# Performance work log

Hardware: AMD Instinct MI355X
Metric: run time of the kernel (lower is better)

Reference implementation:

```python
import jax, jax.numpy as jnp
import numpy as np

N, K, A, LOCAL, PAIR = 1024, 48, 5, 512, 128
RBF_BINS = 16

def _normalize(v, eps=1e-8):
    return v / jnp.sqrt(jnp.sum(v * v, axis=-1, keepdims=True) + eps)

def _frames(pos):
    # pos: (N, A, 3); backbone frame from N(0), CA(1), C(2) via Gram-Schmidt
    n, ca, c = pos[:, 0], pos[:, 1], pos[:, 2]
    e1 = _normalize(c - ca)
    v2 = n - ca
    e2 = _normalize(v2 - jnp.sum(v2 * e1, -1, keepdims=True) * e1)
    e3 = jnp.cross(e1, e2)
    R = jnp.stack([e1, e2, e3], axis=-1)  # (N,3,3) columns are frame axes
    return R, ca

def _rbf(d, d_min=0.0, d_max=22.0, bins=RBF_BINS):
    centers = jnp.linspace(d_min, d_max, bins)
    step = (d_max - d_min) / bins
    return jnp.exp(-((d[..., None] - centers) / step) ** 2)

def setup_inputs():
    key = jax.random.key(0)
    ks = jax.random.split(key, 16)
    def rn(k, shape, scale=1.0):
        return (scale * jax.random.normal(k, shape)).astype(jnp.float32)
    local = rn(ks[0], (N, LOCAL))
    pos = rn(ks[1], (N, A, 3), 3.0)
    pair = rn(ks[2], (N, N, PAIR), 0.1)
    neighbours = jax.random.randint(ks[3], (N, K), 0, N).astype(jnp.int32)
    mask = jnp.ones((N,), dtype=bool)
    d_dist = A * A * RBF_BINS   # 400
    d_dir = A * A * 3           # 75
    d_vec = 2 * A * 3           # 30
    s = lambda f: 1.0 / np.sqrt(f)
    return dict(
        local=local, pos=pos, pair=pair, neighbours=neighbours, mask=mask,
        W_li=rn(ks[4], (LOCAL, PAIR), s(LOCAL)),
        W_lj=rn(ks[5], (LOCAL, PAIR), s(LOCAL)),
        W_dist=rn(ks[6], (d_dist, PAIR), s(d_dist)),
        W_dir=rn(ks[7], (d_dir, PAIR), s(d_dir)),
        W_rot=rn(ks[8], (9, PAIR), s(9)),
        W_vec=rn(ks[9], (d_vec, PAIR), s(d_vec)),
        ln_scale=jnp.ones((PAIR,), jnp.float32),
        ln_bias=jnp.zeros((PAIR,), jnp.float32),
        mlp_w1=rn(ks[10], (PAIR, 2 * PAIR), s(PAIR)),
        mlp_b1=jnp.zeros((2 * PAIR,), jnp.float32),
        mlp_w2=rn(ks[11], (2 * PAIR, PAIR), s(2 * PAIR)),
        mlp_b2=jnp.zeros((PAIR,), jnp.float32),
    )

def reference(local, pos, pair, neighbours, mask,
              W_li, W_lj, W_dist, W_dir, W_rot, W_vec,
              ln_scale, ln_bias, mlp_w1, mlp_b1, mlp_w2, mlp_b2):
    n_idx = jnp.arange(neighbours.shape[0])
    pair_mask = (mask[:, None] & mask[neighbours]) & (neighbours != -1)
    p = pair[n_idx[:, None], neighbours]                      # (N,K,PAIR) gather
    R, t = _frames(pos)                                       # (N,3,3), (N,3)
    pos_nb = pos[neighbours]                                  # (N,K,A,3)
    # source / target node feature projections
    p = p + (local @ W_li)[:, None] + (local @ W_lj)[neighbours]
    # distance features: all atom-pair distances, RBF-encoded in [0, 22]
    off = pos[:, None, :, None, :] - pos_nb[:, :, None, :, :] # (N,K,A,A,3)
    dist = jnp.sqrt(jnp.sum(off * off, -1) + 1e-8)            # (N,K,A,A)
    p = p + _rbf(dist).reshape(*neighbours.shape, -1) @ W_dist
    # direction features: atom-pair offsets in the local frame, normalized
    off_local = jnp.einsum('nij,nkabi->nkabj', R, off)
    p = p + _normalize(off_local).reshape(*neighbours.shape, -1) @ W_dir
    # relative rotation features: R_i^T R_j, flattened
    R_rel = jnp.einsum('nai,nkaj->nkij', R, R[neighbours])
    p = p + R_rel.reshape(*neighbours.shape, 9) @ W_rot
    # pair vector features: self and neighbour atoms in the local frame (x0.1)
    x_self = jnp.einsum('nij,nai->naj', R, pos - t[:, None])            # (N,A,3)
    x_nb = jnp.einsum('nij,nkai->nkaj', R, pos_nb - t[:, None, None])   # (N,K,A,3)
    vec = jnp.concatenate(
        (0.1 * jnp.broadcast_to(x_self[:, None], x_nb.shape), 0.1 * x_nb),
        axis=-1).reshape(*neighbours.shape, -1)
    p = p + vec @ W_vec
    # LayerNorm (scale + offset)
    mu = jnp.mean(p, -1, keepdims=True)
    var = jnp.var(p, -1, keepdims=True)
    p = (p - mu) * jax.lax.rsqrt(var + 1e-5) * ln_scale + ln_bias
    # MLP: hidden 2*PAIR, gelu, linear out
    p = jax.nn.gelu(p @ mlp_w1 + mlp_b1) @ mlp_w2 + mlp_b2
    return p, pair_mask
```

## Files before the change

### kernel.cpp

```cpp
#include <hip/hip_runtime.h>
#include <hip/hip_bf16.h>
#include <math.h>

#define N 1024
#define K 48
#define A 5
#define LOCALD 512
#define PAIRD 128
#define ROWS 32
#define FEATK 544
#define SF_STRIDE_B 1152

#define WS_LI (N*9 + N*3 + N*15)
#define WS_LJ (WS_LI + N*128)
#define WCT_OFF 1159168u
#define W1T_OFF 1298432u
#define W2T_OFF 1363968u
#define PA_OFF  1429504u
#define WS_NEEDED (1429504ull + 49152ull*128*2)

typedef _Float16 half8 __attribute__((ext_vector_type(8)));
typedef float f32x16 __attribute__((ext_vector_type(16)));

__device__ __forceinline__ float gelu_fast(float x) {
    float u2 = 1.5957691216057308f * x * (1.0f + 0.044715f * x * x);
    float t = __expf(-u2);
    return x * __builtin_amdgcn_rcpf(1.0f + t);
}

__device__ __forceinline__ void frame_from(const float* __restrict__ P, float* __restrict__ R) {
    float e1x = P[6] - P[3], e1y = P[7] - P[4], e1z = P[8] - P[5];
    float inv1 = rsqrtf(e1x * e1x + e1y * e1y + e1z * e1z + 1e-8f);
    e1x *= inv1; e1y *= inv1; e1z *= inv1;
    float v2x = P[0] - P[3], v2y = P[1] - P[4], v2z = P[2] - P[5];
    float dp = v2x * e1x + v2y * e1y + v2z * e1z;
    float e2x = v2x - dp * e1x, e2y = v2y - dp * e1y, e2z = v2z - dp * e1z;
    float inv2 = rsqrtf(e2x * e2x + e2y * e2y + e2z * e2z + 1e-8f);
    e2x *= inv2; e2y *= inv2; e2z *= inv2;
    float e3x = e1y * e2z - e1z * e2y;
    float e3y = e1z * e2x - e1x * e2z;
    float e3z = e1x * e2y - e1y * e2x;
    R[0] = e1x; R[1] = e2x; R[2] = e3x;
    R[3] = e1y; R[4] = e2y; R[5] = e3y;
    R[6] = e1z; R[7] = e2z; R[8] = e3z;
}

__global__ __launch_bounds__(256) void prep_kernel(
    const float* __restrict__ local_,
    const float* __restrict__ W_li, const float* __restrict__ W_lj,
    const float* __restrict__ Wd, const float* __restrict__ Wdir,
    const float* __restrict__ Wrot, const float* __restrict__ Wv,
    const float* __restrict__ w1, const float* __restrict__ w2,
    float* __restrict__ ws, char* __restrict__ wsb)
{
    const int tid = threadIdx.x;
    if (blockIdx.x >= 256) {
        _Float16* wct = (_Float16*)(wsb + WCT_OFF);
        _Float16* w1t = (_Float16*)(wsb + W1T_OFF);
        _Float16* w2t = (_Float16*)(wsb + W2T_OFF);
        int g = (blockIdx.x - 256) * 256 + tid;
        if (g < 128 * 544) {
            int c = g & 127, f = g >> 7;
            float v = 0.0f;
            if (f < 400) v = Wd[(size_t)f * 128 + c];
            else if (f < 475) v = Wdir[(size_t)(f - 400) * 128 + c];
            else if (f < 484) v = Wrot[(size_t)(f - 475) * 128 + c];
            else if (f < 514) v = Wv[(size_t)(f - 484) * 128 + c];
            wct[(size_t)c * FEATK + f] = (_Float16)v;
        } else {
            int g2 = g - 128 * 544;
            if (g2 < 256 * 128) {
                int c = g2 & 255, f = g2 >> 8;
                w1t[(size_t)c * 128 + f] = (_Float16)w1[(size_t)f * 256 + c];
            } else {
                int g3 = g2 - 256 * 128;
                if (g3 < 128 * 256) {
                    int c = g3 & 127, f = g3 >> 7;
                    w2t[(size_t)c * 256 + f] = (_Float16)w2[(size_t)f * 128 + c];
                }
            }
        }
        return;
    }

    const int n0 = blockIdx.x * 4;
    __shared__ float sl[4][LOCALD];
    for (int t = tid; t < 4 * LOCALD; t += 256) {
        int r = t >> 9, q = t & 511;
        sl[r][q] = local_[(size_t)(n0 + r) * LOCALD + q];
    }
    __syncthreads();

    const int c = tid & 127;
    const int hh = tid >> 7;
    const int r0 = hh * 2;
    float ali0 = 0, ali1 = 0, alj0 = 0, alj1 = 0;
    const float* wli = W_li + c;
    const float* wlj = W_lj + c;
    #pragma unroll 8
    for (int f = 0; f < LOCALD; ++f) {
        float a_ = wli[(size_t)f * 128];
        float b_ = wlj[(size_t)f * 128];
        float l0 = sl[r0 + 0][f], l1 = sl[r0 + 1][f];
        ali0 += l0 * a_; ali1 += l1 * a_;
        alj0 += l0 * b_; alj1 += l1 * b_;
    }
    ws[WS_LI + (size_t)(n0 + r0 + 0) * 128 + c] = ali0;
    ws[WS_LI + (size_t)(n0 + r0 + 1) * 128 + c] = ali1;
    ws[WS_LJ + (size_t)(n0 + r0 + 0) * 128 + c] = alj0;
    ws[WS_LJ + (size_t)(n0 + r0 + 1) * 128 + c] = alj1;
}

__device__ __forceinline__ void sfw(char* smem, int r, int f, float v) {
    int off = r * SF_STRIDE_B + ((f * 2) ^ ((r & 7) << 4));
    *(_Float16*)(smem + off) = (_Float16)v;
}

template<bool SPLIT>
__global__ __launch_bounds__(256, 4) void main_kernel(
    const float* __restrict__ pair, const float* __restrict__ pos,
    const int* __restrict__ neigh, const int* __restrict__ mask,
    const float* __restrict__ ln_s, const float* __restrict__ ln_b,
    const float* __restrict__ b1, const float* __restrict__ b2,
    const float* __restrict__ ws, const char* __restrict__ wsb,
    _Float16* __restrict__ pa, float* __restrict__ out)
{
    const int R0 = blockIdx.x * ROWS;
    const int tid = threadIdx.x;
    const int lane = tid & 63;
    const int wv = tid >> 6;
    const int myrow = lane & 31;
    const int hi = lane >> 5;
    const int khalf = hi * 8;
    const int swz = (myrow & 7) << 4;

    __shared__ __align__(16) char smem[40960];
    int*   sn  = (int*)(smem + 36864);
    int*   sj  = (int*)(smem + 36992);
    float* spn = (float*)(smem + 37120);
    float* spj = (float*)(smem + 39040);

    const _Float16* wct = (const _Float16*)(wsb + WCT_OFF);
    const int colbase = wv * 32 + myrow;

    if (tid < ROWS) {
        int Rg = R0 + tid;
        int n = Rg / K;
        int kk = Rg - n * K;
        int j = neigh[n * K + kk];
        if (j < 0) j += N;
        sn[tid] = n; sj[tid] = j;
    }
    __syncthreads();

    const int nb0 = R0 / K;
    const int nb1 = (nb0 + 1 < N) ? nb0 + 1 : nb0;
    float li0 = ws[WS_LI + (size_t)nb0 * PAIRD + colbase];
    float li1 = ws[WS_LI + (size_t)nb1 * PAIRD + colbase];
    float pv[16];
    #pragma unroll
    for (int q = 0; q < 16; ++q) {
        int rr = (q & 3) + 8 * (q >> 2) + 4 * hi;
        int nq = sn[rr], jq = sj[rr];
        float li = (nq == nb0) ? li0 : li1;
        pv[q] = pair[((size_t)nq * N + jq) * PAIRD + colbase]
              + ws[WS_LJ + (size_t)jq * PAIRD + colbase] + li;
    }

    for (int t = tid; t < ROWS * 15; t += 256) {
        int r = t / 15, q = t % 15;
        spn[t] = pos[(size_t)sn[r] * 15 + q];
        spj[t] = pos[(size_t)sj[r] * 15 + q];
    }
    __syncthreads();

    {
        const int fr  = tid >> 3;
        const int sub = tid & 7;
        const float* Pn = spn + fr * 15;
        const float* Pj = spj + fr * 15;

        sfw(smem, fr, 514 + sub, 0.0f);
        sfw(smem, fr, 522 + sub, 0.0f);
        sfw(smem, fr, 530 + sub, 0.0f);
        if (sub < 6) sfw(smem, fr, 538 + sub, 0.0f);

        float rn[9];
        frame_from(Pn, rn);

        #pragma unroll
        for (int m = 0; m < 4; ++m) {
            int ab = sub + 8 * m;
            if (ab < 25) {
                int a = ab / 5, b = ab - 5 * (ab / 5);
                float o0 = Pn[a * 3 + 0] - Pj[b * 3 + 0];
                float o1 = Pn[a * 3 + 1] - Pj[b * 3 + 1];
                float o2 = Pn[a * 3 + 2] - Pj[b * 3 + 2];
                float d = sqrtf(o0 * o0 + o1 * o1 + o2 * o2 + 1e-8f);
                float z = d * (16.0f / 22.0f);
                int base = a * 80 + b * 16;
                int rb = fr * SF_STRIDE_B;
                int rsw = (fr & 7) << 4;
                #pragma unroll
                for (int bp = 0; bp < 8; ++bp) {
                    float e0 = __expf(-z * z);
                    float z1 = z - 1.0666666666666667f;
                    float e1 = __expf(-z1 * z1);
                    z = z1 - 1.0666666666666667f;
                    union { _Float16 h[2]; unsigned u; } pk;
                    pk.h[0] = (_Float16)e0; pk.h[1] = (_Float16)e1;
                    int off = rb + (((base + bp * 2) * 2) ^ rsw);
                    *(unsigned*)(smem + off) = pk.u;
                }
                float l0 = rn[0] * o0 + rn[3] * o1 + rn[6] * o2;
                float l1 = rn[1] * o0 + rn[4] * o1 + rn[7] * o2;
                float l2 = rn[2] * o0 + rn[5] * o1 + rn[8] * o2;
                float inv = rsqrtf(l0 * l0 + l1 * l1 + l2 * l2 + 1e-8f);
                int dbase = 400 + a * 15 + b * 3;
                sfw(smem, fr, dbase + 0, l0 * inv);
                sfw(smem, fr, dbase + 1, l1 * inv);
                sfw(smem, fr, dbase + 2, l2 * inv);
            }
        }

        #pragma unroll
        for (int m = 0; m < 2; ++m) {
            int task = (m == 0) ? sub : (sub < 2 ? 8 + sub : -1);
            if (task >= 0) {
                int a = task >> 1;
                int kind = task & 1;
                const float* Ps = kind ? Pj : Pn;
                float v0 = Ps[a * 3 + 0] - Pn[3];
                float v1 = Ps[a * 3 + 1] - Pn[4];
                float v2 = Ps[a * 3 + 2] - Pn[5];
                float x0 = rn[0] * v0 + rn[3] * v1 + rn[6] * v2;
                float x1 = rn[1] * v0 + rn[4] * v1 + rn[7] * v2;
                float x2 = rn[2] * v0 + rn[5] * v1 + rn[8] * v2;
                int dbase = 484 + a * 6 + kind * 3;
                sfw(smem, fr, dbase + 0, 0.1f * x0);
                sfw(smem, fr, dbase + 1, 0.1f * x1);
                sfw(smem, fr, dbase + 2, 0.1f * x2);
            }
        }

        if (sub == 7) {
            float rj[9];
            frame_from(Pj, rj);
            #pragma unroll
            for (int i = 0; i < 3; ++i)
                #pragma unroll
                for (int jd = 0; jd < 3; ++jd) {
                    float v = rn[0 * 3 + i] * rj[0 * 3 + jd]
                            + rn[1 * 3 + i] * rj[1 * 3 + jd]
                            + rn[2 * 3 + i] * rj[2 * 3 + jd];
                    sfw(smem, fr, 475 + i * 3 + jd, v);
                }
        }
    }
    __syncthreads();

    f32x16 acc0, acc1;
    #pragma unroll
    for (int q = 0; q < 16; ++q) { acc0[q] = 0.0f; acc1[q] = 0.0f; }
    {
        const _Float16* wp = wct + (size_t)colbase * FEATK + khalf;
        #pragma unroll
        for (int ks = 0; ks < 34; ks += 2) {
            half8 b0 = *(const half8*)(wp + ks * 16);
            half8 b1 = *(const half8*)(wp + (ks + 1) * 16);
            int k0 = ks * 16 + khalf;
            int k1 = (ks + 1) * 16 + khalf;
            half8 a0 = *(const half8*)(smem + myrow * SF_STRIDE_B + ((k0 * 2) ^ swz));
            half8 a1 = *(const half8*)(smem + myrow * SF_STRIDE_B + ((k1 * 2) ^ swz));
            acc0 = __builtin_amdgcn_mfma_f32_32x32x16_f16(a0, b0, acc0, 0, 0, 0);
            acc1 = __builtin_amdgcn_mfma_f32_32x32x16_f16(a1, b1, acc1, 0, 0, 0);
        }
    }
    __syncthreads();

    #pragma unroll
    for (int q = 0; q < 16; ++q) {
        int rr = (q & 3) + 8 * (q >> 2) + 4 * hi;
        *(float*)(smem + rr * 512 + colbase * 4) = acc0[q] + acc1[q] + pv[q];
    }
    __syncthreads();

    {
        float lns0 = ln_s[lane], lns1 = ln_s[lane + 64];
        float lnb0 = ln_b[lane], lnb1 = ln_b[lane + 64];
        #pragma unroll
        for (int rr8 = 0; rr8 < 8; ++rr8) {
            int row = wv * 8 + rr8;
            float v0 = *(float*)(smem + row * 512 + lane * 4);
            float v1 = *(float*)(smem + row * 512 + (lane + 64) * 4);
            float s = v0 + v1, s2 = v0 * v0 + v1 * v1;
            #pragma unroll
            for (int o = 32; o > 0; o >>= 1) {
                s += __shfl_xor(s, o, 64);
                s2 += __shfl_xor(s2, o, 64);
            }
            float mu = s * (1.0f / 128.0f);
            float var = s2 * (1.0f / 128.0f) - mu * mu;
            float rs = rsqrtf(var + 1e-5f);
            float y0 = (v0 - mu) * rs * lns0 + lnb0;
            float y1 = (v1 - mu) * rs * lns1 + lnb1;
            if constexpr (SPLIT) {
                pa[(size_t)(R0 + row) * PAIRD + lane]      = (_Float16)y0;
                pa[(size_t)(R0 + row) * PAIRD + lane + 64] = (_Float16)y1;
            } else {
                int sw = (row & 7) << 4;
                *(_Float16*)(smem + 16384 + row * 256 + ((lane * 2) ^ sw)) = (_Float16)y0;
                *(_Float16*)(smem + 16384 + row * 256 + (((lane + 64) * 2) ^ sw)) = (_Float16)y1;
            }
        }
    }
    if constexpr (SPLIT) return;

    __syncthreads();

    {
        const _Float16* w1t = (const _Float16*)(wsb + W1T_OFF);
        const int c0 = wv * 64 + myrow;
        const int c1 = c0 + 32;
        const _Float16* wp0 = w1t + (size_t)c0 * 128 + khalf;
        const _Float16* wp1 = w1t + (size_t)c1 * 128 + khalf;
        f32x16 h0, h1;
        #pragma unroll
        for (int q = 0; q < 16; ++q) { h0[q] = 0.0f; h1[q] = 0.0f; }
        #pragma unroll
        for (int ks = 0; ks < 8; ++ks) {
            half8 wf0 = *(const half8*)(wp0 + ks * 16);
            half8 wf1 = *(const half8*)(wp1 + ks * 16);
            int k0 = ks * 16 + khalf;
            half8 a = *(const half8*)(smem + 16384 + myrow * 256 + ((k0 * 2) ^ swz));
            h0 = __builtin_amdgcn_mfma_f32_32x32x16_f16(a, wf0, h0, 0, 0, 0);
            h1 = __builtin_amdgcn_mfma_f32_32x32x16_f16(a, wf1, h1, 0, 0, 0);
        }
        float bb0 = b1[c0], bb1 = b1[c1];
        #pragma unroll
        for (int q = 0; q < 16; ++q) {
            int rr = (q & 3) + 8 * (q >> 2) + 4 * hi;
            int sw = (rr & 7) << 4;
            *(_Float16*)(smem + rr * 512 + ((c0 * 2) ^ sw)) = (_Float16)gelu_fast(h0[q] + bb0);
            *(_Float16*)(smem + rr * 512 + ((c1 * 2) ^ sw)) = (_Float16)gelu_fast(h1[q] + bb1);
        }
    }
    __syncthreads();

    {
        const _Float16* w2t = (const _Float16*)(wsb + W2T_OFF);
        const int oc = wv * 32 + myrow;
        const _Float16* wp = w2t + (size_t)oc * 256 + khalf;
        f32x16 o0, o1;
        #pragma unroll
        for (int q = 0; q < 16; ++q) { o0[q] = 0.0f; o1[q] = 0.0f; }
        #pragma unroll
        for (int ks = 0; ks < 16; ks += 2) {
            half8 w0 = *(const half8*)(wp + ks * 16);
            half8 w1f = *(const half8*)(wp + (ks + 1) * 16);
            int k0 = ks * 16 + khalf;
            int k1 = (ks + 1) * 16 + khalf;
            half8 a0 = *(const half8*)(smem + myrow * 512 + ((k0 * 2) ^ swz));
            half8 a1 = *(const half8*)(smem + myrow * 512 + ((k1 * 2) ^ swz));
            o0 = __builtin_amdgcn_mfma_f32_32x32x16_f16(a0, w0, o0, 0, 0, 0);
            o1 = __builtin_amdgcn_mfma_f32_32x32x16_f16(a1, w1f, o1, 0, 0, 0);
        }
        float bb = b2[oc];
        #pragma unroll
        for (int q = 0; q < 16; ++q) {
            int rr = (q & 3) + 8 * (q >> 2) + 4 * hi;
            out[((size_t)(R0 + rr)) * PAIRD + oc] = o0[q] + o1[q] + bb;
        }
    }

    if (tid < ROWS) {
        int Rg = R0 + tid;
        int n = Rg / K;
        int kk = Rg - n * K;
        int jr = neigh[n * K + kk];
        int jj = jr < 0 ? jr + N : jr;
        bool pm = (jr != -1) && (mask[n] != 0) && (mask[jj] != 0);
        out[(size_t)N * K * PAIRD + Rg] = pm ? 1.0f : 0.0f;
    }
}

__global__ __launch_bounds__(256, 3) void mlp_kernel(
    const _Float16* __restrict__ pa, const int* __restrict__ neigh,
    const int* __restrict__ mask, const float* __restrict__ b1,
    const float* __restrict__ b2, const char* __restrict__ wsb,
    float* __restrict__ out)
{
    const int R0 = blockIdx.x * 64;
    const int tid = threadIdx.x;
    const int lane = tid & 63;
    const int wv = tid >> 6;
    const int myrow = lane & 31;
    const int hi = lane >> 5;
    const int khalf = hi * 8;
    const int swz = (myrow & 7) << 4;

    __shared__ __align__(16) char smem[49152];

    for (int ch = tid; ch < 1024; ch += 256) {
        int row = ch >> 4, c16 = ch & 15;
        half8 v = *(const half8*)(pa + (size_t)(R0 + row) * PAIRD + c16 * 8);
        *(half8*)(smem + row * 256 + ((c16 * 16) ^ ((row & 7) << 4))) = v;
    }
    __syncthreads();

    {
        const _Float16* w1t = (const _Float16*)(wsb + W1T_OFF);
        const int c0 = wv * 64 + myrow;
        const int c1 = c0 + 32;
        const _Float16* wp0 = w1t + (size_t)c0 * 128 + khalf;
        const _Float16* wp1 = w1t + (size_t)c1 * 128 + khalf;
        f32x16 h00, h01, h10, h11;
        #pragma unroll
        for (int q = 0; q < 16; ++q) { h00[q] = 0.0f; h01[q] = 0.0f; h10[q] = 0.0f; h11[q] = 0.0f; }
        #pragma unroll
        for (int ks = 0; ks < 8; ++ks) {
            int k0 = ks * 16 + khalf;
            half8 wf0 = *(const half8*)(wp0 + ks * 16);
            half8 wf1 = *(const half8*)(wp1 + ks * 16);
            half8 a0 = *(const half8*)(smem + myrow * 256 + ((k0 * 2) ^ swz));
            half8 a1 = *(const half8*)(smem + (32 + myrow) * 256 + ((k0 * 2) ^ swz));
            h00 = __builtin_amdgcn_mfma_f32_32x32x16_f16(a0, wf0, h00, 0, 0, 0);
            h01 = __builtin_amdgcn_mfma_f32_32x32x16_f16(a0, wf1, h01, 0, 0, 0);
            h10 = __builtin_amdgcn_mfma_f32_32x32x16_f16(a1, wf0, h10, 0, 0, 0);
            h11 = __builtin_amdgcn_mfma_f32_32x32x16_f16(a1, wf1, h11, 0, 0, 0);
        }
        float bb0 = b1[c0], bb1 = b1[c1];
        #pragma unroll
        for (int q = 0; q < 16; ++q) {
            int rr = (q & 3) + 8 * (q >> 2) + 4 * hi;
            int sw = (rr & 7) << 4;
            *(_Float16*)(smem + 16384 + rr * 512 + ((c0 * 2) ^ sw)) = (_Float16)gelu_fast(h00[q] + bb0);
            *(_Float16*)(smem + 16384 + rr * 512 + ((c1 * 2) ^ sw)) = (_Float16)gelu_fast(h01[q] + bb1);
            *(_Float16*)(smem + 16384 + (rr + 32) * 512 + ((c0 * 2) ^ sw)) = (_Float16)gelu_fast(h10[q] + bb0);
            *(_Float16*)(smem + 16384 + (rr + 32) * 512 + ((c1 * 2) ^ sw)) = (_Float16)gelu_fast(h11[q] + bb1);
        }
    }
    __syncthreads();

    {
        const _Float16* w2t = (const _Float16*)(wsb + W2T_OFF);
        const int oc = wv * 32 + myrow;
        const _Float16* wp = w2t + (size_t)oc * 256 + khalf;
        f32x16 o0, o1;
        #pragma unroll
        for (int q = 0; q < 16; ++q) { o0[q] = 0.0f; o1[q] = 0.0f; }
        #pragma unroll
        for (int ks = 0; ks < 16; ++ks) {
            int k0 = ks * 16 + khalf;
            half8 wf = *(const half8*)(wp + ks * 16);
            half8 a0 = *(const half8*)(smem + 16384 + myrow * 512 + ((k0 * 2) ^ swz));
            half8 a1 = *(const half8*)(smem + 16384 + (32 + myrow) * 512 + ((k0 * 2) ^ swz));
            o0 = __builtin_amdgcn_mfma_f32_32x32x16_f16(a0, wf, o0, 0, 0, 0);
            o1 = __builtin_amdgcn_mfma_f32_32x32x16_f16(a1, wf, o1, 0, 0, 0);
        }
        float bb = b2[oc];
        #pragma unroll
        for (int q = 0; q < 16; ++q) {
            int rr = (q & 3) + 8 * (q >> 2) + 4 * hi;
            out[((size_t)(R0 + rr)) * PAIRD + oc]      = o0[q] + bb;
            out[((size_t)(R0 + rr + 32)) * PAIRD + oc] = o1[q] + bb;
        }
    }

    if (tid < 64) {
        int Rg = R0 + tid;
        int n = Rg / K;
        int kk = Rg - n * K;
        int jr = neigh[n * K + kk];
        int jj = jr < 0 ? jr + N : jr;
        bool pm = (jr != -1) && (mask[n] != 0) && (mask[jj] != 0);
        out[(size_t)N * K * PAIRD + Rg] = pm ? 1.0f : 0.0f;
    }
}

extern "C" void kernel_launch(void* const* d_in, const int* in_sizes, int n_in,
                              void* d_out, int out_size, void* d_ws, size_t ws_size,
                              hipStream_t stream) {
    const float* local_ = (const float*)d_in[0];
    const float* pos = (const float*)d_in[1];
    const float* pair = (const float*)d_in[2];
    const int* neigh = (const int*)d_in[3];
    const int* mask = (const int*)d_in[4];
    const float* W_li = (const float*)d_in[5];
    const float* W_lj = (const float*)d_in[6];
    const float* W_dist = (const float*)d_in[7];
    const float* W_dir = (const float*)d_in[8];
    const float* W_rot = (const float*)d_in[9];
    const float* W_vec = (const float*)d_in[10];
    const float* ln_s = (const float*)d_in[11];
    const float* ln_b = (const float*)d_in[12];
    const float* w1 = (const float*)d_in[13];
    const float* b1 = (const float*)d_in[14];
    const float* w2 = (const float*)d_in[15];
    const float* b2 = (const float*)d_in[16];
    float* ws = (float*)d_ws;
    char* wsb = (char*)d_ws;
    _Float16* pa = (_Float16*)(wsb + PA_OFF);
    float* out = (float*)d_out;

    hipLaunchKernelGGL(prep_kernel, dim3(256 + 528), dim3(256), 0, stream,
                       local_, W_li, W_lj, W_dist, W_dir, W_rot, W_vec,
                       w1, w2, ws, wsb);
    if (ws_size >= WS_NEEDED) {
        main_kernel<true><<<dim3((N * K) / ROWS), dim3(256), 0, stream>>>(
            pair, pos, neigh, mask, ln_s, ln_b, b1, b2, ws, wsb, pa, out);
        mlp_kernel<<<dim3((N * K) / 64), dim3(256), 0, stream>>>(
            pa, neigh, mask, b1, b2, wsb, out);
    } else {
        main_kernel<false><<<dim3((N * K) / ROWS), dim3(256), 0, stream>>>(
            pair, pos, neigh, mask, ln_s, ln_b, b1, b2, ws, wsb, pa, out);
    }
}
```

Measured before the change: 80.09 us.

## Keep weight fragments in registers and loop blocks over multiple row tiles

Both the feature-projection kernel and the MLP kernel now load their weight fragments into registers once per block and then process several row tiles in a loop (3 tiles for main, 2 for mlp). Grid sizes shrink to match. This removes repeated global/L2 reads of the weights for every 32/64-row tile. In exchange it uses many more VGPRs (34 half8 fragments in main), so main_kernel's launch bound drops to 2 blocks per CU, and fewer, longer blocks reduce latency hiding and parallelism.

```diff
diff --git a/kernel.cpp b/kernel.cpp
--- a/kernel.cpp
+++ b/kernel.cpp
@@ -8,6 +8,8 @@
 #define LOCALD 512
 #define PAIRD 128
 #define ROWS 32
+#define TPB 3
+#define MTPB 2
 #define FEATK 544
 #define SF_STRIDE_B 1152
 
@@ -117,7 +119,7 @@
 }
 
 template<bool SPLIT>
-__global__ __launch_bounds__(256, 4) void main_kernel(
+__global__ __launch_bounds__(256, 2) void main_kernel(
     const float* __restrict__ pair, const float* __restrict__ pos,
     const int* __restrict__ neigh, const int* __restrict__ mask,
     const float* __restrict__ ln_s, const float* __restrict__ ln_b,
@@ -125,7 +127,6 @@
     const float* __restrict__ ws, const char* __restrict__ wsb,
     _Float16* __restrict__ pa, float* __restrict__ out)
 {
-    const int R0 = blockIdx.x * ROWS;
     const int tid = threadIdx.x;
     const int lane = tid & 63;
     const int wv = tid >> 6;
@@ -140,257 +141,270 @@
     float* spn = (float*)(smem + 37120);
     float* spj = (float*)(smem + 39040);
 
-    const _Float16* wct = (const _Float16*)(wsb + WCT_OFF);
     const int colbase = wv * 32 + myrow;
 
-    if (tid < ROWS) {
-        int Rg = R0 + tid;
-        int n = Rg / K;
-        int kk = Rg - n * K;
-        int j = neigh[n * K + kk];
-        if (j < 0) j += N;
-        sn[tid] = n; sj[tid] = j;
-    }
-    __syncthreads();
-
-    const int nb0 = R0 / K;
-    const int nb1 = (nb0 + 1 < N) ? nb0 + 1 : nb0;
-    float li0 = ws[WS_LI + (size_t)nb0 * PAIRD + colbase];
-    float li1 = ws[WS_LI + (size_t)nb1 * PAIRD + colbase];
-    float pv[16];
-    #pragma unroll
-    for (int q = 0; q < 16; ++q) {
-        int rr = (q & 3) + 8 * (q >> 2) + 4 * hi;
-        int nq = sn[rr], jq = sj[rr];
-        float li = (nq == nb0) ? li0 : li1;
-        pv[q] = pair[((size_t)nq * N + jq) * PAIRD + colbase]
-              + ws[WS_LJ + (size_t)jq * PAIRD + colbase] + li;
-    }
-
-    for (int t = tid; t < ROWS * 15; t += 256) {
-        int r = t / 15, q = t % 15;
-        spn[t] = pos[(size_t)sn[r] * 15 + q];
-        spj[t] = pos[(size_t)sj[r] * 15 + q];
-    }
-    __syncthreads();
-
+    half8 bw[34];
     {
-        const int fr  = tid >> 3;
-        const int sub = tid & 7;
-        const float* Pn = spn + fr * 15;
-        const float* Pj = spj + fr * 15;
-
-        sfw(smem, fr, 514 + sub, 0.0f);
-        sfw(smem, fr, 522 + sub, 0.0f);
-        sfw(smem, fr, 530 + sub, 0.0f);
-        if (sub < 6) sfw(smem, fr, 538 + sub, 0.0f);
-
-        float rn[9];
-        frame_from(Pn, rn);
-
-        #pragma unroll
-        for (int m = 0; m < 4; ++m) {
-            int ab = sub + 8 * m;
-            if (ab < 25) {
-                int a = ab / 5, b = ab - 5 * (ab / 5);
-                float o0 = Pn[a * 3 + 0] - Pj[b * 3 + 0];
-                float o1 = Pn[a * 3 + 1] - Pj[b * 3 + 1];
-                float o2 = Pn[a * 3 + 2] - Pj[b * 3 + 2];
-                float d = sqrtf(o0 * o0 + o1 * o1 + o2 * o2 + 1e-8f);
-                float z = d * (16.0f / 22.0f);
-                int base = a * 80 + b * 16;
-                int rb = fr * SF_STRIDE_B;
-                int rsw = (fr & 7) << 4;
+        const _Float16* wp = (const _Float16*)(wsb + WCT_OFF) + (size_t)colbase * FEATK + khalf;
+        #pragma unroll
+        for (int ks = 0; ks < 34; ++ks)
+            bw[ks] = *(const half8*)(wp + ks * 16);
+    }
+
+    for (int tile = 0; tile < TPB; ++tile) {
+        const int R0 = (blockIdx.x * TPB + tile) * ROWS;
+        __syncthreads();
+
+        if (tid < ROWS) {
+            int Rg = R0 + tid;
+            int n = Rg / K;
+            int kk = Rg - n * K;
+            int j = neigh[n * K + kk];
+            if (j < 0) j += N;
+            sn[tid] = n; sj[tid] = j;
+        }
+        __syncthreads();
+
+        const int nb0 = R0 / K;
+        const int nb1 = (nb0 + 1 < N) ? nb0 + 1 : nb0;
+        float li0 = ws[WS_LI + (size_t)nb0 * PAIRD + colbase];
+        float li1 = ws[WS_LI + (size_t)nb1 * PAIRD + colbase];
+        float pv[16];
+        #pragma unroll
+        for (int q = 0; q < 16; ++q) {
+            int rr = (q & 3) + 8 * (q >> 2) + 4 * hi;
+            int nq = sn[rr], jq = sj[rr];
+            float li = (nq == nb0) ? li0 : li1;
+            pv[q] = pair[((size_t)nq * N + jq) * PAIRD + colbase]
+                  + ws[WS_LJ + (size_t)jq * PAIRD + colbase] + li;
+        }
+
+        for (int t = tid; t < ROWS * 15; t += 256) {
+            int r = t / 15, q = t % 15;
+            spn[t] = pos[(size_t)sn[r] * 15 + q];
+            spj[t] = pos[(size_t)sj[r] * 15 + q];
+        }
+        __syncthreads();
+
+        {
+            const int fr  = tid >> 3;
+            const int sub = tid & 7;
+            const float* Pn = spn + fr * 15;
+            const float* Pj = spj + fr * 15;
+
+            sfw(smem, fr, 514 + sub, 0.0f);
+            sfw(smem, fr, 522 + sub, 0.0f);
+            sfw(smem, fr, 530 + sub, 0.0f);
+            if (sub < 6) sfw(smem, fr, 538 + sub, 0.0f);
+
+            float rn[9];
+            frame_from(Pn, rn);
+
+            #pragma unroll
+            for (int m = 0; m < 4; ++m) {
+                int ab = sub + 8 * m;
+                if (ab < 25) {
+                    int a = ab / 5, b = ab - 5 * (ab / 5);
+                    float o0 = Pn[a * 3 + 0] - Pj[b * 3 + 0];
+                    float o1 = Pn[a * 3 + 1] - Pj[b * 3 + 1];
+                    float o2 = Pn[a * 3 + 2] - Pj[b * 3 + 2];
+                    float d = sqrtf(o0 * o0 + o1 * o1 + o2 * o2 + 1e-8f);
+                    float z = d * (16.0f / 22.0f);
+                    int base = a * 80 + b * 16;
+                    int rb = fr * SF_STRIDE_B;
+                    int rsw = (fr & 7) << 4;
+                    #pragma unroll
+                    for (int bp = 0; bp < 8; ++bp) {
+                        float e0 = __expf(-z * z);
+                        float z1 = z - 1.0666666666666667f;
+                        float e1 = __expf(-z1 * z1);
+                        z = z1 - 1.0666666666666667f;
+                        union { _Float16 h[2]; unsigned u; } pk;
+                        pk.h[0] = (_Float16)e0; pk.h[1] = (_Float16)e1;
+                        int off = rb + (((base + bp * 2) * 2) ^ rsw);
+                        *(unsigned*)(smem + off) = pk.u;
+                    }
+                    float l0 = rn[0] * o0 + rn[3] * o1 + rn[6] * o2;
+                    float l1 = rn[1] * o0 + rn[4] * o1 + rn[7] * o2;
+                    float l2 = rn[2] * o0 + rn[5] * o1 + rn[8] * o2;
+                    float inv = rsqrtf(l0 * l0 + l1 * l1 + l2 * l2 + 1e-8f);
+                    int dbase = 400 + a * 15 + b * 3;
+                    sfw(smem, fr, dbase + 0, l0 * inv);
+                    sfw(smem, fr, dbase + 1, l1 * inv);
+                    sfw(smem, fr, dbase + 2, l2 * inv);
+                }
+            }
+
+            #pragma unroll
+            for (int m = 0; m < 2; ++m) {
+                int task = (m == 0) ? sub : (sub < 2 ? 8 + sub : -1);
+                if (task >= 0) {
+                    int a = task >> 1;
+                    int kind = task & 1;
+                    const float* Ps = kind ? Pj : Pn;
+                    float v0 = Ps[a * 3 + 0] - Pn[3];
+                    float v1 = Ps[a * 3 + 1] - Pn[4];
+                    float v2 = Ps[a * 3 + 2] - Pn[5];
+                    float x0 = rn[0] * v0 + rn[3] * v1 + rn[6] * v2;
+                    float x1 = rn[1] * v0 + rn[4] * v1 + rn[7] * v2;
+                    float x2 = rn[2] * v0 + rn[5] * v1 + rn[8] * v2;
+                    int dbase = 484 + a * 6 + kind * 3;
+                    sfw(smem, fr, dbase + 0, 0.1f * x0);
+                    sfw(smem, fr, dbase + 1, 0.1f * x1);
+                    sfw(smem, fr, dbase + 2, 0.1f * x2);
+                }
+            }
+
+            if (sub == 7) {
+                float rj[9];
+                frame_from(Pj, rj);
                 #pragma unroll
-                for (int bp = 0; bp < 8; ++bp) {
-                    float e0 = __expf(-z * z);
-                    float z1 = z - 1.0666666666666667f;
-                    float e1 = __expf(-z1 * z1);
-                    z = z1 - 1.0666666666666667f;
-                    union { _Float16 h[2]; unsigned u; } pk;
-                    pk.h[0] = (_Float16)e0; pk.h[1] = (_Float16)e1;
-                    int off = rb + (((base + bp * 2) * 2) ^ rsw);
-                    *(unsigned*)(smem + off) = pk.u;
-                }
-                float l0 = rn[0] * o0 + rn[3] * o1 + rn[6] * o2;
-                float l1 = rn[1] * o0 + rn[4] * o1 + rn[7] * o2;
-                float l2 = rn[2] * o0 + rn[5] * o1 + rn[8] * o2;
-                float inv = rsqrtf(l0 * l0 + l1 * l1 + l2 * l2 + 1e-8f);
-                int dbase = 400 + a * 15 + b * 3;
-                sfw(smem, fr, dbase + 0, l0 * inv);
-                sfw(smem, fr, dbase + 1, l1 * inv);
-                sfw(smem, fr, dbase + 2, l2 * inv);
-            }
-        }
-
-        #pragma unroll
-        for (int m = 0; m < 2; ++m) {
-            int task = (m == 0) ? sub : (sub < 2 ? 8 + sub : -1);
-            if (task >= 0) {
-                int a = task >> 1;
-                int kind = task & 1;
-                const float* Ps = kind ? Pj : Pn;
-                float v0 = Ps[a * 3 + 0] - Pn[3];
-                float v1 = Ps[a * 3 + 1] - Pn[4];
-                float v2 = Ps[a * 3 + 2] - Pn[5];
-                float x0 = rn[0] * v0 + rn[3] * v1 + rn[6] * v2;
-                float x1 = rn[1] * v0 + rn[4] * v1 + rn[7] * v2;
-                float x2 = rn[2] * v0 + rn[5] * v1 + rn[8] * v2;
-                int dbase = 484 + a * 6 + kind * 3;
-                sfw(smem, fr, dbase + 0, 0.1f * x0);
-                sfw(smem, fr, dbase + 1, 0.1f * x1);
-                sfw(smem, fr, dbase + 2, 0.1f * x2);
-            }
-        }
-
-        if (sub == 7) {
-            float rj[9];
-            frame_from(Pj, rj);
-            #pragma unroll
-            for (int i = 0; i < 3; ++i)
-                #pragma unroll
-                for (int jd = 0; jd < 3; ++jd) {
-                    float v = rn[0 * 3 + i] * rj[0 * 3 + jd]
-                            + rn[1 * 3 + i] * rj[1 * 3 + jd]
-                            + rn[2 * 3 + i] * rj[2 * 3 + jd];
-                    sfw(smem, fr, 475 + i * 3 + jd, v);
-                }
-        }
-    }
-    __syncthreads();
-
-    f32x16 acc0, acc1;
-    #pragma unroll
-    for (int q = 0; q < 16; ++q) { acc0[q] = 0.0f; acc1[q] = 0.0f; }
-    {
-        const _Float16* wp = wct + (size_t)colbase * FEATK + khalf;
+                for (int i = 0; i < 3; ++i)
+                    #pragma unroll
+                    for (int jd = 0; jd < 3; ++jd) {
+                        float v = rn[0 * 3 + i] * rj[0 * 3 + jd]
+                                + rn[1 * 3 + i] * rj[1 * 3 + jd]
+                                + rn[2 * 3 + i] * rj[2 * 3 + jd];
+                        sfw(smem, fr, 475 + i * 3 + jd, v);
+                    }
+            }
+        }
+        __syncthreads();
+
+        f32x16 acc0, acc1;
+        #pragma unroll
+        for (int q = 0; q < 16; ++q) { acc0[q] = 0.0f; acc1[q] = 0.0f; }
         #pragma unroll
         for (int ks = 0; ks < 34; ks += 2) {
-            half8 b0 = *(const half8*)(wp + ks * 16);
-            half8 b1 = *(const half8*)(wp + (ks + 1) * 16);
             int k0 = ks * 16 + khalf;
             int k1 = (ks + 1) * 16 + khalf;
             half8 a0 = *(const half8*)(smem + myrow * SF_STRIDE_B + ((k0 * 2) ^ swz));
             half8 a1 = *(const half8*)(smem + myrow * SF_STRIDE_B + ((k1 * 2) ^ swz));
-            acc0 = __builtin_amdgcn_mfma_f32_32x32x16_f16(a0, b0, acc0, 0, 0, 0);
-            acc1 = __builtin_amdgcn_mfma_f32_32x32x16_f16(a1, b1, acc1, 0, 0, 0);
-        }
-    }
-    __syncthreads();
-
-    #pragma unroll
-    for (int q = 0; q < 16; ++q) {
-        int rr = (q & 3) + 8 * (q >> 2) + 4 * hi;
-        *(float*)(smem + rr * 512 + colbase * 4) = acc0[q] + acc1[q] + pv[q];
-    }
-    __syncthreads();
-
-    {
-        float lns0 = ln_s[lane], lns1 = ln_s[lane + 64];
-        float lnb0 = ln_b[lane], lnb1 = ln_b[lane + 64];
-        #pragma unroll
-        for (int rr8 = 0; rr8 < 8; ++rr8) {
-            int row = wv * 8 + rr8;
-            float v0 = *(float*)(smem + row * 512 + lane * 4);
-            float v1 = *(float*)(smem + row * 512 + (lane + 64) * 4);
-            float s = v0 + v1, s2 = v0 * v0 + v1 * v1;
-            #pragma unroll
-            for (int o = 32; o > 0; o >>= 1) {
-                s += __shfl_xor(s, o, 64);
-                s2 += __shfl_xor(s2, o, 64);
-            }
-            float mu = s * (1.0f / 128.0f);
-            float var = s2 * (1.0f / 128.0f) - mu * mu;
-            float rs = rsqrtf(var + 1e-5f);
-            float y0 = (v0 - mu) * rs * lns0 + lnb0;
-            float y1 = (v1 - mu) * rs * lns1 + lnb1;
-            if constexpr (SPLIT) {
-                pa[(size_t)(R0 + row) * PAIRD + lane]      = (_Float16)y0;
-                pa[(size_t)(R0 + row) * PAIRD + lane + 64] = (_Float16)y1;
-            } else {
-                int sw = (row & 7) << 4;
-                *(_Float16*)(smem + 16384 + row * 256 + ((lane * 2) ^ sw)) = (_Float16)y0;
-                *(_Float16*)(smem + 16384 + row * 256 + (((lane + 64) * 2) ^ sw)) = (_Float16)y1;
-            }
-        }
-    }
-    if constexpr (SPLIT) return;
-
-    __syncthreads();
-
-    {
-        const _Float16* w1t = (const _Float16*)(wsb + W1T_OFF);
-        const int c0 = wv * 64 + myrow;
-        const int c1 = c0 + 32;
-        const _Float16* wp0 = w1t + (size_t)c0 * 128 + khalf;
-        const _Float16* wp1 = w1t + (size_t)c1 * 128 + khalf;
-        f32x16 h0, h1;
-        #pragma unroll
-        for (int q = 0; q < 16; ++q) { h0[q] = 0.0f; h1[q] = 0.0f; }
-        #pragma unroll
-        for (int ks = 0; ks < 8; ++ks) {
-            half8 wf0 = *(const half8*)(wp0 + ks * 16);
-            half8 wf1 = *(const half8*)(wp1 + ks * 16);
-            int k0 = ks * 16 + khalf;
-            half8 a = *(const half8*)(smem + 16384 + myrow * 256 + ((k0 * 2) ^ swz));
-            h0 = __builtin_amdgcn_mfma_f32_32x32x16_f16(a, wf0, h0, 0, 0, 0);
-            h1 = __builtin_amdgcn_mfma_f32_32x32x16_f16(a, wf1, h1, 0, 0, 0);
-        }
-        float bb0 = b1[c0], bb1 = b1[c1];
+            acc0 = __builtin_amdgcn_mfma_f32_32x32x16_f16(a0, bw[ks], acc0, 0, 0, 0);
+            acc1 = __builtin_amdgcn_mfma_f32_32x32x16_f16(a1, bw[ks + 1], acc1, 0, 0, 0);
+        }
+        __syncthreads();
+
         #pragma unroll
         for (int q = 0; q < 16; ++q) {
             int rr = (q & 3) + 8 * (q >> 2) + 4 * hi;
-            int sw = (rr & 7) << 4;
-            *(_Float16*)(smem + rr * 512 + ((c0 * 2) ^ sw)) = (_Float16)gelu_fast(h0[q] + bb0);
-            *(_Float16*)(smem + rr * 512 + ((c1 * 2) ^ sw)) = (_Float16)gelu_fast(h1[q] + bb1);
-        }
-    }
-    __syncthreads();
-
-    {
-        const _Float16* w2t = (const _Float16*)(wsb + W2T_OFF);
-        const int oc = wv * 32 + myrow;
-        const _Float16* wp = w2t + (size_t)oc * 256 + khalf;
-        f32x16 o0, o1;
-        #pragma unroll
-        for (int q = 0; q < 16; ++q) { o0[q] = 0.0f; o1[q] = 0.0f; }
-        #pragma unroll
-        for (int ks = 0; ks < 16; ks += 2) {
-            half8 w0 = *(const half8*)(wp + ks * 16);
-            half8 w1f = *(const half8*)(wp + (ks + 1) * 16);
-            int k0 = ks * 16 + khalf;
-            int k1 = (ks + 1) * 16 + khalf;
-            half8 a0 = *(const half8*)(smem + myrow * 512 + ((k0 * 2) ^ swz));
-            half8 a1 = *(const half8*)(smem + myrow * 512 + ((k1 * 2) ^ swz));
-            o0 = __builtin_amdgcn_mfma_f32_32x32x16_f16(a0, w0, o0, 0, 0, 0);
-            o1 = __builtin_amdgcn_mfma_f32_32x32x16_f16(a1, w1f, o1, 0, 0, 0);
-        }
-        float bb = b2[oc];
-        #pragma unroll
-        for (int q = 0; q < 16; ++q) {
-            int rr = (q & 3) + 8 * (q >> 2) + 4 * hi;
-            out[((size_t)(R0 + rr)) * PAIRD + oc] = o0[q] + o1[q] + bb;
-        }
-    }
-
-    if (tid < ROWS) {
-        int Rg = R0 + tid;
-        int n = Rg / K;
-        int kk = Rg - n * K;
-        int jr = neigh[n * K + kk];
-        int jj = jr < 0 ? jr + N : jr;
-        bool pm = (jr != -1) && (mask[n] != 0) && (mask[jj] != 0);
-        out[(size_t)N * K * PAIRD + Rg] = pm ? 1.0f : 0.0f;
-    }
-}
-
-__global__ __launch_bounds__(256, 3) void mlp_kernel(
+            *(float*)(smem + rr * 512 + colbase * 4) = acc0[q] + acc1[q] + pv[q];
+        }
+        __syncthreads();
+
+        {
+            float lns0 = ln_s[lane], lns1 = ln_s[lane + 64];
+            float lnb0 = ln_b[lane], lnb1 = ln_b[lane + 64];
+            #pragma unroll
+            for (int rr8 = 0; rr8 < 8; ++rr8) {
+                int row = wv * 8 + rr8;
+                float v0 = *(float*)(smem + row * 512 + lane * 4);
+                float v1 = *(float*)(smem + row * 512 + (lane + 64) * 4);
+                float s = v0 + v1, s2 = v0 * v0 + v1 * v1;
+                #pragma unroll
+                for (int o = 32; o > 0; o >>= 1) {
+                    s += __shfl_xor(s, o, 64);
+                    s2 += __shfl_xor(s2, o, 64);
+                }
+                float mu = s * (1.0f / 128.0f);
+                float var = s2 * (1.0f / 128.0f) - mu * mu;
+                float rs = rsqrtf(var + 1e-5f);
+                float y0 = (v0 - mu) * rs * lns0 + lnb0;
+                float y1 = (v1 - mu) * rs * lns1 + lnb1;
+                if constexpr (SPLIT) {
+                    *(_Float16*)(smem + 16384 + row * 256 + lane * 2) = (_Float16)y0;
+                    *(_Float16*)(smem + 16384 + row * 256 + (lane + 64) * 2) = (_Float16)y1;
+                } else {
+                    int sw = (row & 7) << 4;
+                    *(_Float16*)(smem + 16384 + row * 256 + ((lane * 2) ^ sw)) = (_Float16)y0;
+                    *(_Float16*)(smem + 16384 + row * 256 + (((lane + 64) * 2) ^ sw)) = (_Float16)y1;
+                }
+            }
+        }
+        __syncthreads();
+
+        if constexpr (SPLIT) {
+            for (int ch = tid; ch < ROWS * 16; ch += 256) {
+                int row = ch >> 4, c16 = ch & 15;
+                half8 v = *(const half8*)(smem + 16384 + row * 256 + c16 * 16);
+                *(half8*)(pa + (size_t)(R0 + row) * PAIRD + c16 * 8) = v;
+            }
+            continue;
+        }
+
+        {
+            const _Float16* w1t = (const _Float16*)(wsb + W1T_OFF);
+            const int c0 = wv * 64 + myrow;
+            const int c1 = c0 + 32;
+            const _Float16* wp0 = w1t + (size_t)c0 * 128 + khalf;
+            const _Float16* wp1 = w1t + (size_t)c1 * 128 + khalf;
+            f32x16 h0, h1;
+            #pragma unroll
+            for (int q = 0; q < 16; ++q) { h0[q] = 0.0f; h1[q] = 0.0f; }
+            #pragma unroll
+            for (int ks = 0; ks < 8; ++ks) {
+                half8 wf0 = *(const half8*)(wp0 + ks * 16);
+                half8 wf1 = *(const half8*)(wp1 + ks * 16);
+                int k0 = ks * 16 + khalf;
+                half8 a = *(const half8*)(smem + 16384 + myrow * 256 + ((k0 * 2) ^ swz));
+                h0 = __builtin_amdgcn_mfma_f32_32x32x16_f16(a, wf0, h0, 0, 0, 0);
+                h1 = __builtin_amdgcn_mfma_f32_32x32x16_f16(a, wf1, h1, 0, 0, 0);
+            }
+            float bb0 = b1[c0], bb1 = b1[c1];
+            #pragma unroll
+            for (int q = 0; q < 16; ++q) {
+                int rr = (q & 3) + 8 * (q >> 2) + 4 * hi;
+                int sw = (rr & 7) << 4;
+                *(_Float16*)(smem + rr * 512 + ((c0 * 2) ^ sw)) = (_Float16)gelu_fast(h0[q] + bb0);
+                *(_Float16*)(smem + rr * 512 + ((c1 * 2) ^ sw)) = (_Float16)gelu_fast(h1[q] + bb1);
+            }
+        }
+        __syncthreads();
+
+        {
+            const _Float16* w2t = (const _Float16*)(wsb + W2T_OFF);
+            const int oc = wv * 32 + myrow;
+            const _Float16* wp = w2t + (size_t)oc * 256 + khalf;
+            f32x16 o0, o1;
+            #pragma unroll
+            for (int q = 0; q < 16; ++q) { o0[q] = 0.0f; o1[q] = 0.0f; }
+            #pragma unroll
+            for (int ks = 0; ks < 16; ks += 2) {
+                half8 w0 = *(const half8*)(wp + ks * 16);
+                half8 w1f = *(const half8*)(wp + (ks + 1) * 16);
+                int k0 = ks * 16 + khalf;
+                int k1 = (ks + 1) * 16 + khalf;
+                half8 a0 = *(const half8*)(smem + myrow * 512 + ((k0 * 2) ^ swz));
+                half8 a1 = *(const half8*)(smem + myrow * 512 + ((k1 * 2) ^ swz));
+                o0 = __builtin_amdgcn_mfma_f32_32x32x16_f16(a0, w0, o0, 0, 0, 0);
+                o1 = __builtin_amdgcn_mfma_f32_32x32x16_f16(a1, w1f, o1, 0, 0, 0);
+            }
+            float bb = b2[oc];
+            #pragma unroll
+            for (int q = 0; q < 16; ++q) {
+                int rr = (q & 3) + 8 * (q >> 2) + 4 * hi;
+                out[((size_t)(R0 + rr)) * PAIRD + oc] = o0[q] + o1[q] + bb;
+            }
+        }
+
+        if (tid < ROWS) {
+            int Rg = R0 + tid;
+            int n = Rg / K;
+            int kk = Rg - n * K;
+            int jr = neigh[n * K + kk];
+            int jj = jr < 0 ? jr + N : jr;
+            bool pm = (jr != -1) && (mask[n] != 0) && (mask[jj] != 0);
+            out[(size_t)N * K * PAIRD + Rg] = pm ? 1.0f : 0.0f;
+        }
+    }
+}
+
+__global__ __launch_bounds__(256, 2) void mlp_kernel(
     const _Float16* __restrict__ pa, const int* __restrict__ neigh,
     const int* __restrict__ mask, const float* __restrict__ b1,
     const float* __restrict__ b2, const char* __restrict__ wsb,
     float* __restrict__ out)
 {
-    const int R0 = blockIdx.x * 64;
     const int tid = threadIdx.x;
     const int lane = tid & 63;
     const int wv = tid >> 6;
@@ -401,80 +415,93 @@
 
     __shared__ __align__(16) char smem[49152];
 
-    for (int ch = tid; ch < 1024; ch += 256) {
-        int row = ch >> 4, c16 = ch & 15;
-        half8 v = *(const half8*)(pa + (size_t)(R0 + row) * PAIRD + c16 * 8);
-        *(half8*)(smem + row * 256 + ((c16 * 16) ^ ((row & 7) << 4))) = v;
-    }
-    __syncthreads();
-
+    const int c0 = wv * 64 + myrow;
+    const int c1 = c0 + 32;
+    const int oc = wv * 32 + myrow;
+    half8 wf0[8], wf1[8], w2f[16];
     {
         const _Float16* w1t = (const _Float16*)(wsb + W1T_OFF);
-        const int c0 = wv * 64 + myrow;
-        const int c1 = c0 + 32;
+        const _Float16* w2t = (const _Float16*)(wsb + W2T_OFF);
         const _Float16* wp0 = w1t + (size_t)c0 * 128 + khalf;
         const _Float16* wp1 = w1t + (size_t)c1 * 128 + khalf;
-        f32x16 h00, h01, h10, h11;
-        #pragma unroll
-        for (int q = 0; q < 16; ++q) { h00[q] = 0.0f; h01[q] = 0.0f; h10[q] = 0.0f; h11[q] = 0.0f; }
+        const _Float16* wp2 = w2t + (size_t)oc * 256 + khalf;
         #pragma unroll
         for (int ks = 0; ks < 8; ++ks) {
-            int k0 = ks * 16 + khalf;
-            half8 wf0 = *(const half8*)(wp0 + ks * 16);
-            half8 wf1 = *(const half8*)(wp1 + ks * 16);
-            half8 a0 = *(const half8*)(smem + myrow * 256 + ((k0 * 2) ^ swz));
-            half8 a1 = *(const half8*)(smem + (32 + myrow) * 256 + ((k0 * 2) ^ swz));
-            h00 = __builtin_amdgcn_mfma_f32_32x32x16_f16(a0, wf0, h00, 0, 0, 0);
-            h01 = __builtin_amdgcn_mfma_f32_32x32x16_f16(a0, wf1, h01, 0, 0, 0);
-            h10 = __builtin_amdgcn_mfma_f32_32x32x16_f16(a1, wf0, h10, 0, 0, 0);
-            h11 = __builtin_amdgcn_mfma_f32_32x32x16_f16(a1, wf1, h11, 0, 0, 0);
-        }
-        float bb0 = b1[c0], bb1 = b1[c1];
-        #pragma unroll
-        for (int q = 0; q < 16; ++q) {
-            int rr = (q & 3) + 8 * (q >> 2) + 4 * hi;
-            int sw = (rr & 7) << 4;
-            *(_Float16*)(smem + 16384 + rr * 512 + ((c0 * 2) ^ sw)) = (_Float16)gelu_fast(h00[q] + bb0);
-            *(_Float16*)(smem + 16384 + rr * 512 + ((c1 * 2) ^ sw)) = (_Float16)gelu_fast(h01[q] + bb1);
-            *(_Float16*)(smem + 16384 + (rr + 32) * 512 + ((c0 * 2) ^ sw)) = (_Float16)gelu_fast(h10[q] + bb0);
-            *(_Float16*)(smem + 16384 + (rr + 32) * 512 + ((c1 * 2) ^ sw)) = (_Float16)gelu_fast(h11[q] + bb1);
-        }
-    }
-    __syncthreads();
-
-    {
-        const _Float16* w2t = (const _Float16*)(wsb + W2T_OFF);
-        const int oc = wv * 32 + myrow;
-        const _Float16* wp = w2t + (size_t)oc * 256 + khalf;
-        f32x16 o0, o1;
-        #pragma unroll
-        for (int q = 0; q < 16; ++q) { o0[q] = 0.0f; o1[q] = 0.0f; }
-        #pragma unroll
-        for (int ks = 0; ks < 16; ++ks) {
-            int k0 = ks * 16 + khalf;
-            half8 wf = *(const half8*)(wp + ks * 16);
-            half8 a0 = *(const half8*)(smem + 16384 + myrow * 512 + ((k0 * 2) ^ swz));
-            half8 a1 = *(const half8*)(smem + 16384 + (32 + myrow) * 512 + ((k0 * 2) ^ swz));
-            o0 = __builtin_amdgcn_mfma_f32_32x32x16_f16(a0, wf, o0, 0, 0, 0);
-            o1 = __builtin_amdgcn_mfma_f32_32x32x16_f16(a1, wf, o1, 0, 0, 0);
-        }
-        float bb = b2[oc];
-        #pragma unroll
-        for (int q = 0; q < 16; ++q) {
-            int rr = (q & 3) + 8 * (q >> 2) + 4 * hi;
-            out[((size_t)(R0 + rr)) * PAIRD + oc]      = o0[q] + bb;
-            out[((size_t)(R0 + rr + 32)) * PAIRD + oc] = o1[q] + bb;
-        }
-    }
-
-    if (tid < 64) {
-        int Rg = R0 + tid;
-        int n = Rg / K;
-        int kk = Rg - n * K;
-        int jr = neigh[n * K + kk];
-        int jj = jr < 0 ? jr + N : jr;
-        bool pm = (jr != -1) && (mask[n] != 0) && (mask[jj] != 0);
-        out[(size_t)N * K * PAIRD + Rg] = pm ? 1.0f : 0.0f;
+            wf0[ks] = *(const half8*)(wp0 + ks * 16);
+            wf1[ks] = *(const half8*)(wp1 + ks * 16);
+        }
+        #pragma unroll
+        for (int ks = 0; ks < 16; ++ks)
+            w2f[ks] = *(const half8*)(wp2 + ks * 16);
+    }
+    const float bb0 = b1[c0], bb1 = b1[c1], bb2 = b2[oc];
+
+    for (int tile = 0; tile < MTPB; ++tile) {
+        const int R0 = (blockIdx.x * MTPB + tile) * 64;
+        __syncthreads();
+
+        for (int ch = tid; ch < 1024; ch += 256) {
+            int row = ch >> 4, c16 = ch & 15;
+            half8 v = *(const half8*)(pa + (size_t)(R0 + row) * PAIRD + c16 * 8);
+            *(half8*)(smem + row * 256 + ((c16 * 16) ^ ((row & 7) << 4))) = v;
+        }
+        __syncthreads();
+
+        {
+            f32x16 h00, h01, h10, h11;
+            #pragma unroll
+            for (int q = 0; q < 16; ++q) { h00[q] = 0.0f; h01[q] = 0.0f; h10[q] = 0.0f; h11[q] = 0.0f; }
+            #pragma unroll
+            for (int ks = 0; ks < 8; ++ks) {
+                int k0 = ks * 16 + khalf;
+                half8 a0 = *(const half8*)(smem + myrow * 256 + ((k0 * 2) ^ swz));
+                half8 a1 = *(const half8*)(smem + (32 + myrow) * 256 + ((k0 * 2) ^ swz));
+                h00 = __builtin_amdgcn_mfma_f32_32x32x16_f16(a0, wf0[ks], h00, 0, 0, 0);
+                h01 = __builtin_amdgcn_mfma_f32_32x32x16_f16(a0, wf1[ks], h01, 0, 0, 0);
+                h10 = __builtin_amdgcn_mfma_f32_32x32x16_f16(a1, wf0[ks], h10, 0, 0, 0);
+                h11 = __builtin_amdgcn_mfma_f32_32x32x16_f16(a1, wf1[ks], h11, 0, 0, 0);
+            }
+            #pragma unroll
+            for (int q = 0; q < 16; ++q) {
+                int rr = (q & 3) + 8 * (q >> 2) + 4 * hi;
+                int sw = (rr & 7) << 4;
+                *(_Float16*)(smem + 16384 + rr * 512 + ((c0 * 2) ^ sw)) = (_Float16)gelu_fast(h00[q] + bb0);
+                *(_Float16*)(smem + 16384 + rr * 512 + ((c1 * 2) ^ sw)) = (_Float16)gelu_fast(h01[q] + bb1);
+                *(_Float16*)(smem + 16384 + (rr + 32) * 512 + ((c0 * 2) ^ sw)) = (_Float16)gelu_fast(h10[q] + bb0);
+                *(_Float16*)(smem + 16384 + (rr + 32) * 512 + ((c1 * 2) ^ sw)) = (_Float16)gelu_fast(h11[q] + bb1);
+            }
+        }
+        __syncthreads();
+
+        {
+            f32x16 o0, o1;
+            #pragma unroll
+            for (int q = 0; q < 16; ++q) { o0[q] = 0.0f; o1[q] = 0.0f; }
+            #pragma unroll
+            for (int ks = 0; ks < 16; ++ks) {
+                int k0 = ks * 16 + khalf;
+                half8 a0 = *(const half8*)(smem + 16384 + myrow * 512 + ((k0 * 2) ^ swz));
+                half8 a1 = *(const half8*)(smem + 16384 + (32 + myrow) * 512 + ((k0 * 2) ^ swz));
+                o0 = __builtin_amdgcn_mfma_f32_32x32x16_f16(a0, w2f[ks], o0, 0, 0, 0);
+                o1 = __builtin_amdgcn_mfma_f32_32x32x16_f16(a1, w2f[ks], o1, 0, 0, 0);
+            }
+            #pragma unroll
+            for (int q = 0; q < 16; ++q) {
+                int rr = (q & 3) + 8 * (q >> 2) + 4 * hi;
+                out[((size_t)(R0 + rr)) * PAIRD + oc]      = o0[q] + bb2;
+                out[((size_t)(R0 + rr + 32)) * PAIRD + oc] = o1[q] + bb2;
+            }
+        }
+
+        if (tid < 64) {
+            int Rg = R0 + tid;
+            int n = Rg / K;
+            int kk = Rg - n * K;
+            int jr = neigh[n * K + kk];
+            int jj = jr < 0 ? jr + N : jr;
+            bool pm = (jr != -1) && (mask[n] != 0) && (mask[jj] != 0);
+            out[(size_t)N * K * PAIRD + Rg] = pm ? 1.0f : 0.0f;
+        }
     }
 }
 
@@ -507,12 +534,12 @@
                        local_, W_li, W_lj, W_dist, W_dir, W_rot, W_vec,
                        w1, w2, ws, wsb);
     if (ws_size >= WS_NEEDED) {
-        main_kernel<true><<<dim3((N * K) / ROWS), dim3(256), 0, stream>>>(
+        main_kernel<true><<<dim3((N * K) / (ROWS * TPB)), dim3(256), 0, stream>>>(
             pair, pos, neigh, mask, ln_s, ln_b, b1, b2, ws, wsb, pa, out);
-        mlp_kernel<<<dim3((N * K) / 64), dim3(256), 0, stream>>>(
+        mlp_kernel<<<dim3((N * K) / (64 * MTPB)), dim3(256), 0, stream>>>(
             pa, neigh, mask, b1, b2, wsb, out);
     } else {
-        main_kernel<false><<<dim3((N * K) / ROWS), dim3(256), 0, stream>>>(
+        main_kernel<false><<<dim3((N * K) / (ROWS * TPB)), dim3(256), 0, stream>>>(
             pair, pos, neigh, mask, ln_s, ln_b, b1, b2, ws, wsb, pa, out);
     }
 }
```

After: 156.8 us. +95.8%, slower.
